# Kernel tuning notes

Measured on AMD Instinct MI355X. Metric: run time of the kernel, lower is better.

Reference implementation:

```python
import jax, jax.numpy as jnp
import numpy as np

B, T, D, H = 8, 4096, 256, 256

def setup_inputs() -> dict:
    key = jax.random.key(0)
    ks = jax.random.split(key, 6)
    scale = 1.0 / np.sqrt(D)
    return {
        "x": jax.random.normal(ks[0], (B, T, D), dtype=jnp.float32),
        "h0": jax.random.normal(ks[1], (B, H), dtype=jnp.float32),
        "Wz": jax.random.normal(ks[2], (H, D), dtype=jnp.float32) * scale,
        "bz": jax.random.normal(ks[3], (H,), dtype=jnp.float32) * scale,
        "Wh": jax.random.normal(ks[4], (H, D), dtype=jnp.float32) * scale,
        "bh": jax.random.normal(ks[5], (H,), dtype=jnp.float32) * scale,
    }

def reference(x, h0, Wz, bz, Wh, bh):
    # gate and update depend only on the input (minGRU): compute in one shot
    gate = jax.nn.sigmoid(jnp.einsum("btd,hd->bth", x, Wz) + bz)   # [B,T,H]
    update = jnp.einsum("btd,hd->bth", x, Wh) + bh                  # [B,T,H]

    def step(h, gu):
        g, u = gu
        h_new = (1.0 - g) * h + g * u
        return h_new, h_new

    # scan over time; xs laid out [T,B,H]
    _, hs = jax.lax.scan(step, h0, (jnp.swapaxes(gate, 0, 1), jnp.swapaxes(update, 0, 1)))
    return jnp.swapaxes(hs, 0, 1)  # [B,T,H]
```

## Files before the change

kernel.cpp:

```cpp
#include <hip/hip_runtime.h>
#include <hip/hip_fp16.h>


namespace {
constexpr int kB  = 8;
constexpr int kT  = 4096;
constexpr int kD  = 256;
constexpr int kH  = 256;
constexpr int kBT = kB * kT;

constexpr int TM  = 128;
constexpr int TH  = 64;
constexpr int BK  = 128;
constexpr int kNT = kT / TM;
constexpr int kNChain = kB * (kH / TH);
constexpr int EPS = 66;
}

typedef short s16x8 __attribute__((ext_vector_type(8)));
typedef short s16x4 __attribute__((ext_vector_type(4)));
typedef float f32x4 __attribute__((ext_vector_type(4)));

__device__ __forceinline__ short f2bf(float f) {
    union { float f; unsigned int u; } v; v.f = f;
    unsigned int r = v.u + 0x7fffu + ((v.u >> 16) & 1u);
    return (short)(r >> 16);
}

__device__ __forceinline__ void load_lds16(const void* g, void* l) {
    __builtin_amdgcn_global_load_lds(
        (const __attribute__((address_space(1))) void*)g,
        (__attribute__((address_space(3))) void*)l, 16, 0, 0);
}

__global__ __launch_bounds__(256)
void prologue(const float* __restrict__ x,
              const float* __restrict__ Wz,
              const float* __restrict__ Wh,
              unsigned short* __restrict__ xb,
              unsigned short* __restrict__ wzb,
              unsigned short* __restrict__ whb,
              float4* __restrict__ aggz)
{
    constexpr int X4 = kBT * kD / 4;
    constexpr int W4 = kH  * kD / 4;
    const int i = blockIdx.x * 256 + threadIdx.x;

    if (i >= X4 + 2 * W4) {
        float4 z; z.x = 0.f; z.y = 0.f; z.z = 0.f; z.w = 0.f;
        aggz[i - (X4 + 2 * W4)] = z;
        return;
    }
    const float* src; unsigned short* dst; int j;
    if (i < X4)           { src = x;  dst = xb;  j = i; }
    else if (i < X4 + W4) { src = Wz; dst = wzb; j = i - X4; }
    else                  { src = Wh; dst = whb; j = i - X4 - W4; }
    const float4 v = ((const float4*)src)[j];
    s16x4 p;
    p[0] = f2bf(v.x); p[1] = f2bf(v.y); p[2] = f2bf(v.z); p[3] = f2bf(v.w);
    ((s16x4*)dst)[j] = p;
}

__global__ __launch_bounds__(256, 4)
void gemm_scan_fused(const unsigned short* __restrict__ xb,
                     const unsigned short* __restrict__ wzb,
                     const unsigned short* __restrict__ whb,
                     const float* __restrict__ bz,
                     const float* __restrict__ bh,
                     const float* __restrict__ h0,
                     unsigned long long* __restrict__ agg,
                     float* __restrict__ out)
{
    __shared__ __align__(16) unsigned char smem[36096];
    unsigned short* Xs = (unsigned short*)smem;
    __half* a_lds   = (__half*)smem;
    __half* b_lds   = a_lds + 128 * EPS;
    float2* sub_lds = (float2*)(smem + 33792);
    float*  hs_lds  = (float*)(smem + 35840);

    const int tid  = threadIdx.x;
    const int lane = tid & 63;
    const int wv   = tid >> 6;
    const int ln15 = lane & 15;
    const int quad = lane >> 4;
    const int wr0  = (wv & 1) * 64;
    const int wc0  = (wv >> 1) * 32;

    const int chain = blockIdx.x;
    const int t     = blockIdx.y;
    const int b     = chain >> 2;
    const int col0  = (chain & 3) * TH;
    const int row0  = b * kT + t * TM;

    const int srow4 = lane >> 4;
    const int slot  = lane & 15;

    f32x4 accZ[4][2] = {};
    f32x4 accU[4][2] = {};

    for (int k0 = 0; k0 < kD; k0 += BK) {
        #pragma unroll
        for (int s = 0; s < 8; ++s) {
            const int seg = wv * 8 + s;
            const int m   = seg * 4 + srow4;
            const int c   = slot ^ (m & 15);
            load_lds16(xb + (size_t)(row0 + m) * kD + k0 + c * 8,
                       Xs + seg * 512);
        }
        __syncthreads();

        #pragma unroll
        for (int kk = 0; kk < BK; kk += 32) {
            const int cbase = kk >> 3;
            s16x8 af[4];
            #pragma unroll
            for (int mt = 0; mt < 4; ++mt) {
                const int r = wr0 + mt * 16 + ln15;
                af[mt] = *(const s16x8*)&Xs[r * 128 + (((cbase + quad) ^ ln15) << 3)];
            }
            s16x8 bzf[2], buf[2];
            #pragma unroll
            for (int nt = 0; nt < 2; ++nt) {
                const size_t wrow = (size_t)(col0 + wc0 + nt * 16 + ln15) * kD
                                  + k0 + kk + quad * 8;
                bzf[nt] = *(const s16x8*)(wzb + wrow);
                buf[nt] = *(const s16x8*)(whb + wrow);
            }
            #pragma unroll
            for (int mt = 0; mt < 4; ++mt) {
                #pragma unroll
                for (int nt = 0; nt < 2; ++nt) {
                    accZ[mt][nt] = __builtin_amdgcn_mfma_f32_16x16x32_bf16(
                        af[mt], bzf[nt], accZ[mt][nt], 0, 0, 0);
                    accU[mt][nt] = __builtin_amdgcn_mfma_f32_16x16x32_bf16(
                        af[mt], buf[nt], accU[mt][nt], 0, 0, 0);
                }
            }
        }
        __syncthreads();
    }

    #pragma unroll
    for (int nt = 0; nt < 2; ++nt) {
        const int col = col0 + wc0 + nt * 16 + ln15;
        const int lc  = wc0 + nt * 16 + ln15;
        const float bzv = bz[col];
        const float bhv = bh[col];
        #pragma unroll
        for (int mt = 0; mt < 4; ++mt) {
            const int rb = wr0 + mt * 16 + quad * 4;
            #pragma unroll
            for (int r = 0; r < 4; ++r) {
                const float z = accZ[mt][nt][r] + bzv;
                const float g = 1.0f / (1.0f + __expf(-z));
                const float u = accU[mt][nt][r] + bhv;
                a_lds[(rb + r) * EPS + lc] = __float2half_rn(1.0f - g);
                b_lds[(rb + r) * EPS + lc] = __float2half_rn(g * u);
            }
        }
    }
    __syncthreads();

    const int s = tid >> 6;
    const int h = tid & 63;
    {
        float A = 1.0f, Bv = 0.0f;
        #pragma unroll 8
        for (int r = s * 32; r < s * 32 + 32; ++r) {
            const float a  = __half2float(a_lds[r * EPS + h]);
            const float bb = __half2float(b_lds[r * EPS + h]);
            Bv = fmaf(a, Bv, bb);
            A *= a;
        }
        float2 o; o.x = A; o.y = Bv;
        sub_lds[s * 64 + h] = o;
    }
    __syncthreads();

    if (tid < 64) {
        float A = 1.0f, Bv = 0.0f;
        #pragma unroll
        for (int s2 = 0; s2 < 4; ++s2) {
            const float2 g = sub_lds[s2 * 64 + tid];
            Bv = fmaf(g.x, Bv, g.y);
            A *= g.x;
        }
        union { float2 f; unsigned long long u; } pk;
        pk.f.x = A; pk.f.y = Bv;
        pk.u |= 1ull;
        __hip_atomic_store(&agg[(size_t)(chain * kNT + t) * 64 + tid], pk.u,
                           __ATOMIC_RELAXED, __HIP_MEMORY_SCOPE_AGENT);

        float hs = h0[(size_t)b * kH + col0 + tid];
        for (int j0 = 0; j0 < t; j0 += 8) {
            const int nb = (t - j0 < 8) ? (t - j0) : 8;
            unsigned long long u[8];
            #pragma unroll
            for (int q = 0; q < 8; ++q)
                if (q < nb)
                    u[q] = __hip_atomic_load(
                        &agg[(size_t)(chain * kNT + j0 + q) * 64 + tid],
                        __ATOMIC_RELAXED, __HIP_MEMORY_SCOPE_AGENT);
            #pragma unroll
            for (int q = 0; q < 8; ++q) {
                if (q < nb) {
                    while (u[q] == 0ull)
                        u[q] = __hip_atomic_load(
                            &agg[(size_t)(chain * kNT + j0 + q) * 64 + tid],
                            __ATOMIC_RELAXED, __HIP_MEMORY_SCOPE_AGENT);
                    union { unsigned long long u; float2 f; } qk; qk.u = u[q];
                    hs = fmaf(qk.f.x, hs, qk.f.y);
                }
            }
        }
        hs_lds[tid] = hs;
    }
    __syncthreads();

    {
        float hv = hs_lds[h];
        #pragma unroll
        for (int s2 = 0; s2 < s; ++s2) {
            const float2 g = sub_lds[s2 * 64 + h];
            hv = fmaf(g.x, hv, g.y);
        }
        #pragma unroll 8
        for (int r = 0; r < 32; ++r) {
            const int lr = s * 32 + r;
            const float a  = __half2float(a_lds[lr * EPS + h]);
            const float bb = __half2float(b_lds[lr * EPS + h]);
            hv = fmaf(a, hv, bb);
            __builtin_nontemporal_store(hv, &out[(size_t)(row0 + lr) * kH + col0 + h]);
        }
    }
}

extern "C" void kernel_launch(void* const* d_in, const int* in_sizes, int n_in,
                              void* d_out, int out_size, void* d_ws, size_t ws_size,
                              hipStream_t stream)
{
    const float* x  = (const float*)d_in[0];
    const float* h0 = (const float*)d_in[1];
    const float* Wz = (const float*)d_in[2];
    const float* bz = (const float*)d_in[3];
    const float* Wh = (const float*)d_in[4];
    const float* bh = (const float*)d_in[5];
    float* out = (float*)d_out;

    unsigned char* ws = (unsigned char*)d_ws;
    unsigned short* xb  = (unsigned short*)ws;   ws += (size_t)kBT * kD * 2;
    unsigned short* wzb = (unsigned short*)ws;   ws += (size_t)kH * kD * 2;
    unsigned short* whb = (unsigned short*)ws;   ws += (size_t)kH * kD * 2;
    unsigned long long* agg = (unsigned long long*)ws;

    constexpr int PRO_ITEMS = kBT * kD / 4 + 2 * (kH * kD / 4)
                            + kNChain * kNT * TH * 8 / 16;
    prologue<<<PRO_ITEMS / 256, 256, 0, stream>>>(
        x, Wz, Wh, xb, wzb, whb, (float4*)agg);
    gemm_scan_fused<<<dim3(kNChain, kNT), 256, 0, stream>>>(
        xb, wzb, whb, bz, bh, h0, agg, out);
}
```

Baseline: 128.3 us.

## Stage Wz/Wh weight tiles in LDS alongside X with halved K-block

Weight fragments for both GEMMs were previously read straight from global memory by every wave. They are now staged into LDS through global_load_lds, using an XOR swizzle, next to the X tile. BK is halved to 64 so X plus both weight tiles fit in the existing shared buffer. This aims to cut redundant global and L2 weight traffic, at the cost of twice as many K iterations and barriers.

```diff
diff --git a/kernel.cpp b/kernel.cpp
--- a/kernel.cpp
+++ b/kernel.cpp
@@ -11,7 +11,7 @@
 
 constexpr int TM  = 128;
 constexpr int TH  = 64;
-constexpr int BK  = 128;
+constexpr int BK  = 64;
 constexpr int kNT = kT / TM;
 constexpr int kNChain = kB * (kH / TH);
 constexpr int EPS = 66;
@@ -72,7 +72,9 @@
                      float* __restrict__ out)
 {
     __shared__ __align__(16) unsigned char smem[36096];
-    unsigned short* Xs = (unsigned short*)smem;
+    unsigned short* Xs  = (unsigned short*)smem;
+    unsigned short* Wzs = Xs  + 128 * 64;
+    unsigned short* Whs = Wzs + 64 * 64;
     __half* a_lds   = (__half*)smem;
     __half* b_lds   = a_lds + 128 * EPS;
     float2* sub_lds = (float2*)(smem + 33792);
@@ -92,39 +94,46 @@
     const int col0  = (chain & 3) * TH;
     const int row0  = b * kT + t * TM;
 
-    const int srow4 = lane >> 4;
-    const int slot  = lane & 15;
+    const int srow = lane >> 3;
+    const int swslot = (lane & 7) ^ srow;
 
     f32x4 accZ[4][2] = {};
     f32x4 accU[4][2] = {};
 
     for (int k0 = 0; k0 < kD; k0 += BK) {
         #pragma unroll
-        for (int s = 0; s < 8; ++s) {
-            const int seg = wv * 8 + s;
-            const int m   = seg * 4 + srow4;
-            const int c   = slot ^ (m & 15);
-            load_lds16(xb + (size_t)(row0 + m) * kD + k0 + c * 8,
+        for (int s = 0; s < 4; ++s) {
+            const int seg = wv * 4 + s;
+            const int m = seg * 8 + srow;
+            load_lds16(xb + (size_t)(row0 + m) * kD + k0 + swslot * 8,
                        Xs + seg * 512);
         }
+        #pragma unroll
+        for (int s = 0; s < 2; ++s) {
+            const int seg = wv * 2 + s;
+            const int m = seg * 8 + srow;
+            load_lds16(wzb + (size_t)(col0 + m) * kD + k0 + swslot * 8,
+                       Wzs + seg * 512);
+            load_lds16(whb + (size_t)(col0 + m) * kD + k0 + swslot * 8,
+                       Whs + seg * 512);
+        }
         __syncthreads();
 
         #pragma unroll
         for (int kk = 0; kk < BK; kk += 32) {
-            const int cbase = kk >> 3;
-            s16x8 af[4];
+            const int bblk = (kk >> 3) + quad;
+            s16x8 af[4], bzf[2], buf[2];
             #pragma unroll
             for (int mt = 0; mt < 4; ++mt) {
                 const int r = wr0 + mt * 16 + ln15;
-                af[mt] = *(const s16x8*)&Xs[r * 128 + (((cbase + quad) ^ ln15) << 3)];
-            }
-            s16x8 bzf[2], buf[2];
+                af[mt] = *(const s16x8*)&Xs[r * 64 + ((bblk ^ (r & 7)) << 3)];
+            }
             #pragma unroll
             for (int nt = 0; nt < 2; ++nt) {
-                const size_t wrow = (size_t)(col0 + wc0 + nt * 16 + ln15) * kD
-                                  + k0 + kk + quad * 8;
-                bzf[nt] = *(const s16x8*)(wzb + wrow);
-                buf[nt] = *(const s16x8*)(whb + wrow);
+                const int rw = wc0 + nt * 16 + ln15;
+                const int so = (bblk ^ (rw & 7)) << 3;
+                bzf[nt] = *(const s16x8*)&Wzs[rw * 64 + so];
+                buf[nt] = *(const s16x8*)&Whs[rw * 64 + so];
             }
             #pragma unroll
             for (int mt = 0; mt < 4; ++mt) {
```

New measurement: 116.9 us. 8.9% less time.
